# Kernel optimization log

Hardware: AMD Instinct MI355X
Metric: run time of the kernel (lower is better)

Reference implementation:

```python
import jax, jax.numpy as jnp
import numpy as np

N_NODES = 100000
N_EDGES = 640000
D = 128
NEG_SLOPE = 0.01  # torch LeakyReLU default


def leaky_relu(x):
    return jnp.where(x > 0, x, NEG_SLOPE * x)


def gcn_conv(x, src, dst, W, b, n):
    h = x @ W                                                   # [N, d_out]
    deg = jax.ops.segment_sum(jnp.ones_like(dst, dtype=h.dtype), dst, num_segments=n)
    dinv = jnp.where(deg > 0, jax.lax.rsqrt(deg), 0.0)
    w = dinv[src] * dinv[dst]                                   # [E+N]
    msg = h[src] * w[:, None]                                   # [E+N, d_out]
    return jax.ops.segment_sum(msg, dst, num_segments=n) + b


def setup_inputs() -> dict:
    key = jax.random.key(0)
    ks = jax.random.split(key, 8)
    x = jax.random.normal(ks[0], (N_NODES, D), dtype=jnp.float32)
    edge_index = jax.random.randint(ks[1], (2, N_EDGES), 0, N_NODES, dtype=jnp.int64)
    scale = 1.0 / np.sqrt(D)
    W1 = jax.random.normal(ks[2], (D, D), dtype=jnp.float32) * scale
    W2 = jax.random.normal(ks[3], (D, D), dtype=jnp.float32) * scale
    W3 = jax.random.normal(ks[4], (D, D), dtype=jnp.float32) * scale
    b1 = jnp.zeros((D,), dtype=jnp.float32)
    b2 = jnp.zeros((D,), dtype=jnp.float32)
    b3 = jnp.zeros((D,), dtype=jnp.float32)
    return {"x": x, "edge_index": edge_index, "W1": W1, "b1": b1,
            "W2": W2, "b2": b2, "W3": W3, "b3": b3}


def reference(x, edge_index, W1, b1, W2, b2, W3, b3):
    n = x.shape[0]
    loops = jnp.arange(n, dtype=edge_index.dtype)
    src = jnp.concatenate([edge_index[0], loops])
    dst = jnp.concatenate([edge_index[1], loops])
    # module order per __init__: [act, conv] repeated num_layers times
    x = leaky_relu(x)
    x = gcn_conv(x, src, dst, W1, b1, n)
    x = leaky_relu(x)
    x = gcn_conv(x, src, dst, W2, b2, n)
    x = leaky_relu(x)
    x = gcn_conv(x, src, dst, W3, b3, n)
    return x
```

## Files before the change

### kernel.cpp

```cpp
#include <hip/hip_runtime.h>

#define NSLOPE 0.01f
#define DF 128
#define DMAX 32

typedef __attribute__((ext_vector_type(8))) short short8v;
typedef __attribute__((ext_vector_type(16))) float f32x16;

static __device__ __forceinline__ float lrelu(float x) {
    return x > 0.f ? x : NSLOPE * x;
}
static __device__ __forceinline__ unsigned short f2bf(float f) {
    unsigned u = __float_as_uint(f);
    unsigned r = (u + 0x7FFFu + ((u >> 16) & 1u)) >> 16;
    return (unsigned short)r;
}
static __device__ __forceinline__ float bflo(unsigned u) {
    return __uint_as_float(u << 16);
}
static __device__ __forceinline__ float bfhi(unsigned u) {
    return __uint_as_float(u & 0xFFFF0000u);
}


__global__ __launch_bounds__(256) void prep_zero(int* __restrict__ cnt, int zb, int n4,
                                                 const float* __restrict__ W1,
                                                 const float* __restrict__ W2,
                                                 const float* __restrict__ W3,
                                                 unsigned short* __restrict__ Wt1,
                                                 unsigned short* __restrict__ Wt2,
                                                 unsigned short* __restrict__ Wt3) {
    int bid = blockIdx.x;
    if (bid < zb) {
        int i = bid * 256 + threadIdx.x;
        if (i < n4) ((uint4*)cnt)[i] = make_uint4(0, 0, 0, 0);
        return;
    }
    int wb = bid - zb;
    int m = wb >> 6;
    const float* W = m == 0 ? W1 : (m == 1 ? W2 : W3);
    unsigned short* Wt = m == 0 ? Wt1 : (m == 1 ? Wt2 : Wt3);
    int idx = (wb & 63) * 256 + threadIdx.x;
    int k = idx >> 7, nn = idx & 127;
    Wt[nn * 128 + k] = f2bf(W[idx]);
}


__global__ __launch_bounds__(256) void fill_fused(const int* __restrict__ ei,
                                                  int* __restrict__ cnt,
                                                  int* __restrict__ csr,
                                                  unsigned short* __restrict__ Hb,
                                                  int E, int n) {
    int e = blockIdx.x * 256 + threadIdx.x;
    if (e < E) {
        int d = ei[E + e];
        int pos = atomicAdd(&cnt[d], 1);
        if (pos < DMAX) csr[(d << 5) + pos] = ei[e];
    } else if (e - E < DF) {
        Hb[(size_t)n * DF + (e - E)] = 0;
    }
}


template <bool INF32>
__global__ __launch_bounds__(256) void gemm_mfma(const void* __restrict__ Xv,
                                                 const unsigned short* __restrict__ Wt,
                                                 const int* __restrict__ cnt,
                                                 unsigned short* __restrict__ Hb, int n) {
    __shared__ short8v WsC[128 * 16];

    int tid = threadIdx.x;
    int rowbase = blockIdx.x * 128;

    const short8v* Wt8 = (const short8v*)Wt;
#pragma unroll
    for (int i = 0; i < 8; ++i) {
        int idx = i * 256 + tid;
        int r = idx >> 4, s = idx & 15;
        WsC[r * 16 + (s ^ (r & 15))] = Wt8[idx];
    }
    __syncthreads();

    int w = tid >> 6;
    int l = tid & 63;
    int ln = l & 31;
    int half = l >> 5;
    int xrow = rowbase + 32 * w + ln;
    int xrowc = min(xrow, n - 1);
    int rsw = ln & 15;

    short8v bfrag[8];
    if (INF32) {
        const float4* X4 = (const float4*)Xv + (size_t)xrowc * 32;
#pragma unroll
        for (int ks = 0; ks < 8; ++ks) {
            int ch = ks * 2 + half;
            float4 g0 = X4[ch * 2];
            float4 g1 = X4[ch * 2 + 1];
            short8v v;
            v[0] = f2bf(lrelu(g0.x)); v[1] = f2bf(lrelu(g0.y));
            v[2] = f2bf(lrelu(g0.z)); v[3] = f2bf(lrelu(g0.w));
            v[4] = f2bf(lrelu(g1.x)); v[5] = f2bf(lrelu(g1.y));
            v[6] = f2bf(lrelu(g1.z)); v[7] = f2bf(lrelu(g1.w));
            bfrag[ks] = v;
        }
    } else {
        const short8v* X8 = (const short8v*)Xv + (size_t)xrowc * 16;
#pragma unroll
        for (int ks = 0; ks < 8; ++ks)
            bfrag[ks] = X8[ks * 2 + half];
    }

    f32x16 acc[4];
#pragma unroll
    for (int c = 0; c < 4; ++c)
#pragma unroll
        for (int r = 0; r < 16; ++r) acc[c][r] = 0.f;

#pragma unroll
    for (int ks = 0; ks < 8; ++ks) {
        int sw = (ks * 2 + half) ^ rsw;
        short8v a0 = WsC[(0 * 32 + ln) * 16 + sw];
        short8v a1 = WsC[(1 * 32 + ln) * 16 + sw];
        short8v a2 = WsC[(2 * 32 + ln) * 16 + sw];
        short8v a3 = WsC[(3 * 32 + ln) * 16 + sw];
        acc[0] = __builtin_amdgcn_mfma_f32_32x32x16_bf16(a0, bfrag[ks], acc[0], 0, 0, 0);
        acc[1] = __builtin_amdgcn_mfma_f32_32x32x16_bf16(a1, bfrag[ks], acc[1], 0, 0, 0);
        acc[2] = __builtin_amdgcn_mfma_f32_32x32x16_bf16(a2, bfrag[ks], acc[2], 0, 0, 0);
        acc[3] = __builtin_amdgcn_mfma_f32_32x32x16_bf16(a3, bfrag[ks], acc[3], 0, 0, 0);
    }

    if (xrow < n) {
        float dv = rsqrtf((float)(cnt[xrow] + 1));
        unsigned short* rowp = Hb + (size_t)xrow * DF;
#pragma unroll
        for (int c = 0; c < 4; ++c) {
#pragma unroll
            for (int gq = 0; gq < 4; ++gq) {
                uint2 pu;
                pu.x = ((unsigned)f2bf(acc[c][4 * gq + 1] * dv) << 16)
                     |  (unsigned)f2bf(acc[c][4 * gq + 0] * dv);
                pu.y = ((unsigned)f2bf(acc[c][4 * gq + 3] * dv) << 16)
                     |  (unsigned)f2bf(acc[c][4 * gq + 2] * dv);
                *(uint2*)(rowp + c * 32 + 8 * gq + 4 * half) = pu;
            }
        }
    }
}


template <int MODE>
__global__ __launch_bounds__(256) void agg_kernel(const unsigned short* __restrict__ H,
                                                  const int* __restrict__ cnt,
                                                  const int* __restrict__ csr,
                                                  const float* __restrict__ b,
                                                  void* __restrict__ outp, int n) {
    int g = blockIdx.x * 256 + threadIdx.x;
    int v = g >> 4;
    int l = g & 15;
    if (v >= n) return;
    const uint4* H16 = (const uint4*)H;
    int deg = cnt[v];
    float dv = rsqrtf((float)(deg + 1));
    int dc = min(deg, DMAX);
    int base = v << 5;
    uint4 su = H16[(size_t)v * 16 + l];
    float acc0 = bflo(su.x), acc1 = bfhi(su.x);
    float acc2 = bflo(su.y), acc3 = bfhi(su.y);
    float acc4 = bflo(su.z), acc5 = bfhi(su.z);
    float acc6 = bflo(su.w), acc7 = bfhi(su.w);
    for (int j = 0; j < dc; j += 8) {
        int idx[8];
#pragma unroll
        for (int i = 0; i < 8; ++i)
            idx[i] = (j + i < dc) ? csr[base + j + i] : n;
        uint4 u[8];
#pragma unroll
        for (int i = 0; i < 8; ++i)
            u[i] = H16[(size_t)idx[i] * 16 + l];
#pragma unroll
        for (int i = 0; i < 8; ++i) {
            acc0 += bflo(u[i].x); acc1 += bfhi(u[i].x);
            acc2 += bflo(u[i].y); acc3 += bfhi(u[i].y);
            acc4 += bflo(u[i].z); acc5 += bfhi(u[i].z);
            acc6 += bflo(u[i].w); acc7 += bfhi(u[i].w);
        }
    }
    const float4* b4 = (const float4*)b;
    float4 bb0 = b4[l * 2];
    float4 bb1 = b4[l * 2 + 1];
    float r0 = bb0.x + dv * acc0, r1 = bb0.y + dv * acc1;
    float r2 = bb0.z + dv * acc2, r3 = bb0.w + dv * acc3;
    float r4 = bb1.x + dv * acc4, r5 = bb1.y + dv * acc5;
    float r6 = bb1.z + dv * acc6, r7 = bb1.w + dv * acc7;
    if (MODE == 0) {
        r0 = lrelu(r0); r1 = lrelu(r1); r2 = lrelu(r2); r3 = lrelu(r3);
        r4 = lrelu(r4); r5 = lrelu(r5); r6 = lrelu(r6); r7 = lrelu(r7);
        uint4 pu;
        pu.x = ((unsigned)f2bf(r1) << 16) | (unsigned)f2bf(r0);
        pu.y = ((unsigned)f2bf(r3) << 16) | (unsigned)f2bf(r2);
        pu.z = ((unsigned)f2bf(r5) << 16) | (unsigned)f2bf(r4);
        pu.w = ((unsigned)f2bf(r7) << 16) | (unsigned)f2bf(r6);
        ((uint4*)outp)[(size_t)v * 16 + l] = pu;
    } else {
        float4* o4 = (float4*)outp;
        o4[(size_t)v * 32 + l * 2]     = make_float4(r0, r1, r2, r3);
        o4[(size_t)v * 32 + l * 2 + 1] = make_float4(r4, r5, r6, r7);
    }
}

extern "C" void kernel_launch(void* const* d_in, const int* in_sizes, int n_in,
                              void* d_out, int out_size, void* d_ws, size_t ws_size,
                              hipStream_t stream) {
    const float* x = (const float*)d_in[0];
    const int* ei = (const int*)d_in[1];
    const float* W1 = (const float*)d_in[2];
    const float* b1 = (const float*)d_in[3];
    const float* W2 = (const float*)d_in[4];
    const float* b2 = (const float*)d_in[5];
    const float* W3 = (const float*)d_in[6];
    const float* b3 = (const float*)d_in[7];
    float* out = (float*)d_out;

    const int N = in_sizes[0] / DF;
    const int E = in_sizes[1] / 2;

    char* ws = (char*)d_ws;
    size_t off = 0;
    auto alloc = [&](size_t bytes) {
        size_t o = off;
        off = (off + bytes + 15) & ~(size_t)15;
        return o;
    };
    int* cnt              = (int*)(ws + alloc((size_t)(N + 3) / 4 * 16));
    int* csr              = (int*)(ws + alloc((size_t)N * DMAX * 4));
    unsigned short* Hb    = (unsigned short*)(ws + alloc((size_t)(N + 1) * DF * 2));
    unsigned short* A     = (unsigned short*)(ws + alloc((size_t)N * DF * 2));
    unsigned short* Wt1   = (unsigned short*)(ws + alloc((size_t)DF * DF * 2));
    unsigned short* Wt2   = (unsigned short*)(ws + alloc((size_t)DF * DF * 2));
    unsigned short* Wt3   = (unsigned short*)(ws + alloc((size_t)DF * DF * 2));

    int n4 = (N + 3) / 4;
    int zb = (n4 + 255) / 256;
    prep_zero<<<zb + 192, 256, 0, stream>>>(cnt, zb, n4, W1, W2, W3, Wt1, Wt2, Wt3);
    fill_fused<<<(E + DF + 255) / 256, 256, 0, stream>>>(ei, cnt, csr, Hb, E, N);

    int gemm_blocks = (N + 127) / 128;
    int agg_blocks = (N * 16 + 255) / 256;

    gemm_mfma<true><<<gemm_blocks, 256, 0, stream>>>(x, Wt1, cnt, Hb, N);
    agg_kernel<0><<<agg_blocks, 256, 0, stream>>>(Hb, cnt, csr, b1, A, N);
    gemm_mfma<false><<<gemm_blocks, 256, 0, stream>>>(A, Wt2, cnt, Hb, N);
    agg_kernel<0><<<agg_blocks, 256, 0, stream>>>(Hb, cnt, csr, b2, A, N);
    gemm_mfma<false><<<gemm_blocks, 256, 0, stream>>>(A, Wt3, cnt, Hb, N);
    agg_kernel<1><<<agg_blocks, 256, 0, stream>>>(Hb, cnt, csr, b3, out, N);
}
```

Before: 197.8 us.

## Fuse aggregation with next layer's GEMM via shared-memory tile

The intermediate aggregate+GEMM pairs for layers 2 and 3 are merged into one kernel. Each block first aggregates 128 nodes into a swizzled LDS tile, then runs MFMA on that tile against weights read directly from global memory. This removes the bf16 round trip of the intermediate activation through HBM and two kernel launches, and ping-pongs between two H buffers. The trade-off is lower gather parallelism per block (128 nodes handled sequentially in 8 passes), weight fragments no longer staged in LDS, and serialization between the gather and MFMA phases within a block.

```diff
diff --git a/kernel.cpp b/kernel.cpp
--- a/kernel.cpp
+++ b/kernel.cpp
@@ -49,21 +49,23 @@
 __global__ __launch_bounds__(256) void fill_fused(const int* __restrict__ ei,
                                                   int* __restrict__ cnt,
                                                   int* __restrict__ csr,
-                                                  unsigned short* __restrict__ Hb,
+                                                  unsigned short* __restrict__ H1,
+                                                  unsigned short* __restrict__ H2,
                                                   int E, int n) {
     int e = blockIdx.x * 256 + threadIdx.x;
     if (e < E) {
         int d = ei[E + e];
         int pos = atomicAdd(&cnt[d], 1);
         if (pos < DMAX) csr[(d << 5) + pos] = ei[e];
-    } else if (e - E < DF) {
-        Hb[(size_t)n * DF + (e - E)] = 0;
-    }
-}
-
-
-template <bool INF32>
-__global__ __launch_bounds__(256) void gemm_mfma(const void* __restrict__ Xv,
+    } else {
+        int t = e - E;
+        if (t < DF) H1[(size_t)n * DF + t] = 0;
+        else if (t < 2 * DF) H2[(size_t)n * DF + (t - DF)] = 0;
+    }
+}
+
+
+__global__ __launch_bounds__(256) void gemm_mfma(const float* __restrict__ X,
                                                  const unsigned short* __restrict__ Wt,
                                                  const int* __restrict__ cnt,
                                                  unsigned short* __restrict__ Hb, int n) {
@@ -90,25 +92,18 @@
     int rsw = ln & 15;
 
     short8v bfrag[8];
-    if (INF32) {
-        const float4* X4 = (const float4*)Xv + (size_t)xrowc * 32;
-#pragma unroll
-        for (int ks = 0; ks < 8; ++ks) {
-            int ch = ks * 2 + half;
-            float4 g0 = X4[ch * 2];
-            float4 g1 = X4[ch * 2 + 1];
-            short8v v;
-            v[0] = f2bf(lrelu(g0.x)); v[1] = f2bf(lrelu(g0.y));
-            v[2] = f2bf(lrelu(g0.z)); v[3] = f2bf(lrelu(g0.w));
-            v[4] = f2bf(lrelu(g1.x)); v[5] = f2bf(lrelu(g1.y));
-            v[6] = f2bf(lrelu(g1.z)); v[7] = f2bf(lrelu(g1.w));
-            bfrag[ks] = v;
-        }
-    } else {
-        const short8v* X8 = (const short8v*)Xv + (size_t)xrowc * 16;
-#pragma unroll
-        for (int ks = 0; ks < 8; ++ks)
-            bfrag[ks] = X8[ks * 2 + half];
+    const float4* X4 = (const float4*)X + (size_t)xrowc * 32;
+#pragma unroll
+    for (int ks = 0; ks < 8; ++ks) {
+        int ch = ks * 2 + half;
+        float4 g0 = X4[ch * 2];
+        float4 g1 = X4[ch * 2 + 1];
+        short8v v;
+        v[0] = f2bf(lrelu(g0.x)); v[1] = f2bf(lrelu(g0.y));
+        v[2] = f2bf(lrelu(g0.z)); v[3] = f2bf(lrelu(g0.w));
+        v[4] = f2bf(lrelu(g1.x)); v[5] = f2bf(lrelu(g1.y));
+        v[6] = f2bf(lrelu(g1.z)); v[7] = f2bf(lrelu(g1.w));
+        bfrag[ks] = v;
     }
 
     f32x16 acc[4];
@@ -149,12 +144,123 @@
 }
 
 
-template <int MODE>
-__global__ __launch_bounds__(256) void agg_kernel(const unsigned short* __restrict__ H,
-                                                  const int* __restrict__ cnt,
-                                                  const int* __restrict__ csr,
-                                                  const float* __restrict__ b,
-                                                  void* __restrict__ outp, int n) {
+__global__ __launch_bounds__(256) void fused_ag(const unsigned short* __restrict__ Hin,
+                                                const int* __restrict__ cnt,
+                                                const int* __restrict__ csr,
+                                                const float* __restrict__ bias,
+                                                const unsigned short* __restrict__ Wt,
+                                                unsigned short* __restrict__ Hout, int n) {
+    __shared__ uint4 As[128 * 16];
+
+    int tid = threadIdx.x;
+    int rowbase = blockIdx.x * 128;
+    const uint4* H16 = (const uint4*)Hin;
+
+    {
+        int l = tid & 15;
+        const float4* b4 = (const float4*)bias;
+        float4 bb0 = b4[l * 2];
+        float4 bb1 = b4[l * 2 + 1];
+        for (int p = 0; p < 8; ++p) {
+            int vt = p * 16 + (tid >> 4);
+            int vc = min(rowbase + vt, n - 1);
+            int deg = cnt[vc];
+            float dv = rsqrtf((float)(deg + 1));
+            int dc = min(deg, DMAX);
+            int base = vc << 5;
+            uint4 su = H16[(size_t)vc * 16 + l];
+            float acc0 = bflo(su.x), acc1 = bfhi(su.x);
+            float acc2 = bflo(su.y), acc3 = bfhi(su.y);
+            float acc4 = bflo(su.z), acc5 = bfhi(su.z);
+            float acc6 = bflo(su.w), acc7 = bfhi(su.w);
+            for (int j = 0; j < dc; j += 8) {
+                int idx[8];
+#pragma unroll
+                for (int i = 0; i < 8; ++i)
+                    idx[i] = (j + i < dc) ? csr[base + j + i] : n;
+                uint4 u[8];
+#pragma unroll
+                for (int i = 0; i < 8; ++i)
+                    u[i] = H16[(size_t)idx[i] * 16 + l];
+#pragma unroll
+                for (int i = 0; i < 8; ++i) {
+                    acc0 += bflo(u[i].x); acc1 += bfhi(u[i].x);
+                    acc2 += bflo(u[i].y); acc3 += bfhi(u[i].y);
+                    acc4 += bflo(u[i].z); acc5 += bfhi(u[i].z);
+                    acc6 += bflo(u[i].w); acc7 += bfhi(u[i].w);
+                }
+            }
+            float r0 = lrelu(bb0.x + dv * acc0), r1 = lrelu(bb0.y + dv * acc1);
+            float r2 = lrelu(bb0.z + dv * acc2), r3 = lrelu(bb0.w + dv * acc3);
+            float r4 = lrelu(bb1.x + dv * acc4), r5 = lrelu(bb1.y + dv * acc5);
+            float r6 = lrelu(bb1.z + dv * acc6), r7 = lrelu(bb1.w + dv * acc7);
+            uint4 pu;
+            pu.x = ((unsigned)f2bf(r1) << 16) | (unsigned)f2bf(r0);
+            pu.y = ((unsigned)f2bf(r3) << 16) | (unsigned)f2bf(r2);
+            pu.z = ((unsigned)f2bf(r5) << 16) | (unsigned)f2bf(r4);
+            pu.w = ((unsigned)f2bf(r7) << 16) | (unsigned)f2bf(r6);
+            As[vt * 16 + (l ^ (vt & 15))] = pu;
+        }
+    }
+    __syncthreads();
+
+    int w = tid >> 6;
+    int l = tid & 63;
+    int ln = l & 31;
+    int half = l >> 5;
+    int xrow = rowbase + 32 * w + ln;
+    int rsw = ln & 15;
+    int tilerow = 32 * w + ln;
+
+    short8v bfrag[8];
+#pragma unroll
+    for (int ks = 0; ks < 8; ++ks)
+        bfrag[ks] = ((const short8v*)As)[tilerow * 16 + ((ks * 2 + half) ^ rsw)];
+
+    const short8v* Wt8 = (const short8v*)Wt;
+    f32x16 acc[4];
+#pragma unroll
+    for (int c = 0; c < 4; ++c)
+#pragma unroll
+        for (int r = 0; r < 16; ++r) acc[c][r] = 0.f;
+
+#pragma unroll
+    for (int ks = 0; ks < 8; ++ks) {
+        int ch = ks * 2 + half;
+        short8v a0 = Wt8[(0 * 32 + ln) * 16 + ch];
+        short8v a1 = Wt8[(1 * 32 + ln) * 16 + ch];
+        short8v a2 = Wt8[(2 * 32 + ln) * 16 + ch];
+        short8v a3 = Wt8[(3 * 32 + ln) * 16 + ch];
+        acc[0] = __builtin_amdgcn_mfma_f32_32x32x16_bf16(a0, bfrag[ks], acc[0], 0, 0, 0);
+        acc[1] = __builtin_amdgcn_mfma_f32_32x32x16_bf16(a1, bfrag[ks], acc[1], 0, 0, 0);
+        acc[2] = __builtin_amdgcn_mfma_f32_32x32x16_bf16(a2, bfrag[ks], acc[2], 0, 0, 0);
+        acc[3] = __builtin_amdgcn_mfma_f32_32x32x16_bf16(a3, bfrag[ks], acc[3], 0, 0, 0);
+    }
+
+    if (xrow < n) {
+        float dv = rsqrtf((float)(cnt[xrow] + 1));
+        unsigned short* rowp = Hout + (size_t)xrow * DF;
+#pragma unroll
+        for (int c = 0; c < 4; ++c) {
+#pragma unroll
+            for (int gq = 0; gq < 4; ++gq) {
+                uint2 pu;
+                pu.x = ((unsigned)f2bf(acc[c][4 * gq + 1] * dv) << 16)
+                     |  (unsigned)f2bf(acc[c][4 * gq + 0] * dv);
+                pu.y = ((unsigned)f2bf(acc[c][4 * gq + 3] * dv) << 16)
+                     |  (unsigned)f2bf(acc[c][4 * gq + 2] * dv);
+                *(uint2*)(rowp + c * 32 + 8 * gq + 4 * half) = pu;
+            }
+        }
+    }
+}
+
+
+__global__ __launch_bounds__(256) void agg_final(const unsigned short* __restrict__ H,
+                                                 const int* __restrict__ cnt,
+                                                 const int* __restrict__ csr,
+                                                 const float* __restrict__ b,
+                                                 float* __restrict__ outp, int n) {
     int g = blockIdx.x * 256 + threadIdx.x;
     int v = g >> 4;
     int l = g & 15;
@@ -189,24 +295,13 @@
     const float4* b4 = (const float4*)b;
     float4 bb0 = b4[l * 2];
     float4 bb1 = b4[l * 2 + 1];
-    float r0 = bb0.x + dv * acc0, r1 = bb0.y + dv * acc1;
-    float r2 = bb0.z + dv * acc2, r3 = bb0.w + dv * acc3;
-    float r4 = bb1.x + dv * acc4, r5 = bb1.y + dv * acc5;
-    float r6 = bb1.z + dv * acc6, r7 = bb1.w + dv * acc7;
-    if (MODE == 0) {
-        r0 = lrelu(r0); r1 = lrelu(r1); r2 = lrelu(r2); r3 = lrelu(r3);
-        r4 = lrelu(r4); r5 = lrelu(r5); r6 = lrelu(r6); r7 = lrelu(r7);
-        uint4 pu;
-        pu.x = ((unsigned)f2bf(r1) << 16) | (unsigned)f2bf(r0);
-        pu.y = ((unsigned)f2bf(r3) << 16) | (unsigned)f2bf(r2);
-        pu.z = ((unsigned)f2bf(r5) << 16) | (unsigned)f2bf(r4);
-        pu.w = ((unsigned)f2bf(r7) << 16) | (unsigned)f2bf(r6);
-        ((uint4*)outp)[(size_t)v * 16 + l] = pu;
-    } else {
-        float4* o4 = (float4*)outp;
-        o4[(size_t)v * 32 + l * 2]     = make_float4(r0, r1, r2, r3);
-        o4[(size_t)v * 32 + l * 2 + 1] = make_float4(r4, r5, r6, r7);
-    }
+    float4* o4 = (float4*)outp;
+    o4[(size_t)v * 32 + l * 2] =
+        make_float4(bb0.x + dv * acc0, bb0.y + dv * acc1,
+                    bb0.z + dv * acc2, bb0.w + dv * acc3);
+    o4[(size_t)v * 32 + l * 2 + 1] =
+        make_float4(bb1.x + dv * acc4, bb1.y + dv * acc5,
+                    bb1.z + dv * acc6, bb1.w + dv * acc7);
 }
 
 extern "C" void kernel_launch(void* const* d_in, const int* in_sizes, int n_in,
@@ -234,8 +329,8 @@
     };
     int* cnt              = (int*)(ws + alloc((size_t)(N + 3) / 4 * 16));
     int* csr              = (int*)(ws + alloc((size_t)N * DMAX * 4));
-    unsigned short* Hb    = (unsigned short*)(ws + alloc((size_t)(N + 1) * DF * 2));
-    unsigned short* A     = (unsigned short*)(ws + alloc((size_t)N * DF * 2));
+    unsigned short* H1    = (unsigned short*)(ws + alloc((size_t)(N + 1) * DF * 2));
+    unsigned short* H2    = (unsigned short*)(ws + alloc((size_t)(N + 1) * DF * 2));
     unsigned short* Wt1   = (unsigned short*)(ws + alloc((size_t)DF * DF * 2));
     unsigned short* Wt2   = (unsigned short*)(ws + alloc((size_t)DF * DF * 2));
     unsigned short* Wt3   = (unsigned short*)(ws + alloc((size_t)DF * DF * 2));
@@ -243,15 +338,13 @@
     int n4 = (N + 3) / 4;
     int zb = (n4 + 255) / 256;
     prep_zero<<<zb + 192, 256, 0, stream>>>(cnt, zb, n4, W1, W2, W3, Wt1, Wt2, Wt3);
-    fill_fused<<<(E + DF + 255) / 256, 256, 0, stream>>>(ei, cnt, csr, Hb, E, N);
-
-    int gemm_blocks = (N + 127) / 128;
+    fill_fused<<<(E + 2 * DF + 255) / 256, 256, 0, stream>>>(ei, cnt, csr, H1, H2, E, N);
+
+    int tile_blocks = (N + 127) / 128;
     int agg_blocks = (N * 16 + 255) / 256;
 
-    gemm_mfma<true><<<gemm_blocks, 256, 0, stream>>>(x, Wt1, cnt, Hb, N);
-    agg_kernel<0><<<agg_blocks, 256, 0, stream>>>(Hb, cnt, csr, b1, A, N);
-    gemm_mfma<false><<<gemm_blocks, 256, 0, stream>>>(A, Wt2, cnt, Hb, N);
-    agg_kernel<0><<<agg_blocks, 256, 0, stream>>>(Hb, cnt, csr, b2, A, N);
-    gemm_mfma<false><<<gemm_blocks, 256, 0, stream>>>(A, Wt3, cnt, Hb, N);
-    agg_kernel<1><<<agg_blocks, 256, 0, stream>>>(Hb, cnt, csr, b3, out, N);
-}
+    gemm_mfma<<<tile_blocks, 256, 0, stream>>>(x, Wt1, cnt, H1, N);
+    fused_ag<<<tile_blocks, 256, 0, stream>>>(H1, cnt, csr, b1, Wt2, H2, N);
+    fused_ag<<<tile_blocks, 256, 0, stream>>>(H2, cnt, csr, b2, Wt3, H1, N);
+    agg_final<<<agg_blocks, 256, 0, stream>>>(H1, cnt, csr, b3, out, N);
+}
```

Result: slower. 223.5 us (+13.0%).
